# Optimization experiments

Measured on AMD Instinct MI355X. Metric: run time of the kernel, lower is better.

## Reference

```python
import jax, jax.numpy as jnp
import numpy as np

H = 150
PASSES = 5
NSETS = 2
N = 50000
E = 400000
G = 64
SLOPE = 0.01  # torch leaky_relu default


def setup_inputs() -> dict:
    key = jax.random.key(0)
    ks = jax.random.split(key, 20)
    def u(k, shape, fan):
        lim = 1.0 / np.sqrt(fan)
        return jax.random.uniform(k, shape, jnp.float32, -lim, lim)
    return {
        "nodes": jax.random.normal(ks[0], (N, H), jnp.float32),
        "problem_type": jax.random.uniform(ks[1], (G, 1), jnp.float32),
        "edge_W": u(ks[2], (NSETS, H, H), H),
        "edge_b": u(ks[3], (NSETS, H), H),
        "gru_w_ih": u(ks[4], (3 * H, H), H),
        "gru_w_hh": u(ks[5], (3 * H, H), H),
        "gru_b_ih": u(ks[6], (3 * H,), H),
        "gru_b_hh": u(ks[7], (3 * H,), H),
        "fc1_w": u(ks[8], (80, 151), 151),
        "fc1_b": u(ks[9], (80,), 151),
        "fc2_w": u(ks[10], (80, 80), 80),
        "fc2_b": u(ks[11], (80,), 80),
        "fcL_w": u(ks[12], (10, 80), 80),
        "fcL_b": u(ks[13], (10,), 80),
        "edges": jax.random.randint(ks[14], (NSETS, E, 2), 0, N),
        "graph_ids": jnp.sort(jax.random.randint(ks[15], (N,), 0, G)),
        "tbptt": 0,
    }


def _gru_cell(x, h, w_ih, w_hh, b_ih, b_hh):
    gi = x @ w_ih.T + b_ih  # [N, 3H]
    gh = h @ w_hh.T + b_hh
    ir, iz, inn = jnp.split(gi, 3, axis=-1)
    hr, hz, hn = jnp.split(gh, 3, axis=-1)
    r = jax.nn.sigmoid(ir + hr)
    z = jax.nn.sigmoid(iz + hz)
    n = jnp.tanh(inn + r * hn)
    return (1.0 - z) * n + z * h


def reference(nodes, problem_type, edge_W, edge_b, gru_w_ih, gru_w_hh,
              gru_b_ih, gru_b_hh, fc1_w, fc1_b, fc2_w, fc2_b, fcL_w, fcL_b,
              edges, graph_ids, tbptt):
    n_sets = edge_W.shape[0]
    n_graphs = problem_type.shape[0]
    for j in range(PASSES):
        incoming = jnp.zeros_like(nodes)
        for k in range(n_sets):
            src = edges[k, :, 1]
            dst = edges[k, :, 0]
            # NOTE: in the source, the first Linear+leaky_relu result is
            # overwritten; the effective edge message is just the second Linear.
            y = nodes[src] @ edge_W[k].T + edge_b[k]  # [E, H]
            incoming = incoming.at[dst].add(y)
        nodes = _gru_cell(incoming, nodes, gru_w_ih, gru_w_hh, gru_b_ih, gru_b_hh)
        if tbptt == 1 and j < PASSES - 2:
            nodes = jax.lax.stop_gradient(nodes)
    g = jax.ops.segment_sum(nodes, graph_ids, num_segments=n_graphs)  # [G, H]
    g = jnp.log(g)
    g = jnp.where(jnp.isnan(g), 0.0, g)
    g = jax.nn.relu(g)
    x = jnp.concatenate([g, problem_type], axis=1)  # [G, 151]
    x = jax.nn.leaky_relu(x @ fc1_w.T + fc1_b, SLOPE)
    x = jax.nn.leaky_relu(x @ fc2_w.T + fc2_b, SLOPE)
    return x @ fcL_w.T + fcL_b  # [G, 10]
```

## Files before the change

### kernel.cpp

```cpp
#include <hip/hip_runtime.h>
#include <stdint.h>

#define NN 50000
#define H 150
#define NE 400000
#define NG 64
#define NPASS 5
#define KB 480
#define VC 640
#define NRB 391

typedef unsigned short u16;
typedef unsigned int u32;
typedef __attribute__((ext_vector_type(8))) short short8;
typedef __attribute__((ext_vector_type(4))) float float4v;
typedef __attribute__((ext_vector_type(4))) u32 uint4v;

__device__ __forceinline__ u16 f2bf_rn(float x) {
  union { float f; u32 u; } v; v.f = x;
  u32 r = v.u + 0x7fffu + ((v.u >> 16) & 1u);
  return (u16)(r >> 16);
}
__device__ __forceinline__ float bf2f(u16 h) {
  union { u32 u; float f; } v; v.u = ((u32)h) << 16;
  return v.f;
}
__device__ __forceinline__ u32 packf(float v) {
  u16 hi = f2bf_rn(v);
  u16 lo = f2bf_rn(v - bf2f(hi));
  return (u32)hi | ((u32)lo << 16);
}
__device__ __forceinline__ float upk(u32 u) {
  union { u32 u; float f; } a, b;
  a.u = u << 16; b.u = u & 0xffff0000u;
  return a.f + b.f;
}
__device__ __forceinline__ void async16(const void* g, void* l) {
  __builtin_amdgcn_global_load_lds(
      (const __attribute__((address_space(1))) unsigned int*)(uintptr_t)g,
      (__attribute__((address_space(3))) unsigned int*)(uint32_t)(uintptr_t)l,
      16, 0, 0);
}

__global__ void hist_kernel(const int* __restrict__ edges, int* __restrict__ cnt) {
  int id = blockIdx.x * 256 + threadIdx.x;
  if (id >= 2 * NE) return;
  int dst = edges[id * 2];
  int set = id / NE;
  atomicAdd(&cnt[dst * 2 + set], 1);
}

__global__ __launch_bounds__(1024) void scan1_kernel(const int* __restrict__ cnt,
                                                     int* __restrict__ rowptr,
                                                     int* __restrict__ bsum, int n) {
  __shared__ int sd[1024];
  int t = threadIdx.x;
  int idx = blockIdx.x * 1024 + t;
  int v = (idx < n) ? cnt[idx] : 0;
  sd[t] = v;
  __syncthreads();
  for (int off = 1; off < 1024; off <<= 1) {
    int add = (t >= off) ? sd[t - off] : 0;
    __syncthreads();
    sd[t] += add;
    __syncthreads();
  }
  if (idx < n) rowptr[idx] = sd[t] - v;
  if (t == 1023) bsum[blockIdx.x] = sd[1023];
}

__global__ __launch_bounds__(128) void scan2_kernel(const int* __restrict__ bsum,
                                                    int* __restrict__ boff, int nb) {
  __shared__ int sd[128];
  int t = threadIdx.x;
  int v = (t < nb) ? bsum[t] : 0;
  sd[t] = v;
  __syncthreads();
  for (int off = 1; off < 128; off <<= 1) {
    int add = (t >= off) ? sd[t - off] : 0;
    __syncthreads();
    sd[t] += add;
    __syncthreads();
  }
  boff[t] = sd[t] - v;
}

__global__ void scan3_kernel(int* __restrict__ rowptr, const int* __restrict__ boff, int n) {
  int idx = blockIdx.x * 256 + threadIdx.x;
  if (idx < n) rowptr[idx] += boff[idx >> 10];
}

__global__ void total_kernel(int* __restrict__ rowptr, const int* __restrict__ boff, int n, int nb) {
  if (threadIdx.x == 0 && blockIdx.x == 0) rowptr[n] = boff[nb];
}

__global__ void copy_int_kernel(const int* __restrict__ a, int* __restrict__ b, int n) {
  int id = blockIdx.x * 256 + threadIdx.x;
  if (id < n) b[id] = a[id];
}

__global__ void fill_kernel(const int* __restrict__ edges, int* __restrict__ cursor,
                            u16* __restrict__ colbuf) {
  int id = blockIdx.x * 256 + threadIdx.x;
  if (id >= 2 * NE) return;
  int dst = edges[id * 2];
  int src = edges[id * 2 + 1];
  int set = id / NE;
  int pos = atomicAdd(&cursor[dst * 2 + set], 1);
  colbuf[pos] = (u16)src;
}

__global__ void bounds_kernel(const int* __restrict__ gids, int* __restrict__ gstart) {
  int g = threadIdx.x;
  if (g > NG) return;
  int lo = 0, hi = NN;
  while (lo < hi) { int m = (lo + hi) >> 1; if (gids[m] < g) lo = m + 1; else hi = m; }
  gstart[g] = lo;
}

__global__ void build_B_kernel(const float* __restrict__ wih, const float* __restrict__ whh,
                               const float* __restrict__ eW,
                               u16* __restrict__ Bh, u16* __restrict__ Bl) {
  int id = blockIdx.x * 256 + threadIdx.x;
  if (id >= VC * KB) return;
  int v = id / KB, k = id % KB;
  int g = (v >> 4) & 3, c = (v >> 6) * 16 + (v & 15);
  int seg = k / 160, kk = k % 160;
  float val = 0.f;
  if (c < H && kk < H) {
    if (seg < 2) {
      if (g < 3) {
        const float* wr = wih + (size_t)(g * H + c) * H;
        const float* wc = eW + (size_t)seg * H * H + kk;
        float acc = 0.f;
        for (int t = 0; t < H; t++) acc += wr[t] * wc[(size_t)t * H];
        val = acc;
      }
    } else {
      if (g == 0) val = whh[(size_t)c * H + kk];
      else if (g == 1) val = whh[(size_t)(H + c) * H + kk];
      else if (g == 3) val = whh[(size_t)(2 * H + c) * H + kk];
    }
  }
  u16 h = f2bf_rn(val);
  Bh[id] = h;
  Bl[id] = f2bf_rn(val - bf2f(h));
}

__global__ void build_coef_kernel(const float* __restrict__ wih,
                                  const float* __restrict__ eb,
                                  const float* __restrict__ bih, const float* __restrict__ bhh,
                                  float* __restrict__ coefs) {
  int id = threadIdx.x + blockIdx.x * 256;
  if (id >= VC) return;
  int g = id / 160, c = id % 160;
  float u0 = 0.f, u1 = 0.f, bs = 0.f;
  if (c < H) {
    if (g < 3) {
      const float* wr = wih + (size_t)(g * H + c) * H;
      for (int t = 0; t < H; t++) { u0 += wr[t] * eb[t]; u1 += wr[t] * eb[H + t]; }
    }
    if (g == 0) bs = bih[c] + bhh[c];
    else if (g == 1) bs = bih[H + c] + bhh[H + c];
    else if (g == 2) bs = bih[2 * H + c];
    else bs = bhh[2 * H + c];
  }
  coefs[id] = u0;
  coefs[VC + id] = u1;
  coefs[2 * VC + id] = bs;
}

__global__ void init_nodes_kernel(const float* __restrict__ nin,
                                  u32* __restrict__ npkA, u32* __restrict__ npkB) {
  int id = blockIdx.x * 256 + threadIdx.x;
  if (id >= NN * 160) return;
  int r = id / 160, c = id % 160;
  if (c < H) {
    npkA[id] = packf(nin[(size_t)r * H + c]);
  } else {
    npkA[id] = 0;
    npkB[id] = 0;
  }
}

__global__ void pad_S_kernel(u16* __restrict__ Sh, u16* __restrict__ Sl) {
  int id = blockIdx.x * 256 + threadIdx.x;
  if (id >= NN * 20) return;
  int r = id / 20, rem = id % 20;
  int set = rem / 10, t = rem % 10;
  size_t off = (size_t)r * 320 + set * 160 + H + t;
  Sh[off] = 0; Sl[off] = 0;
}

__global__ __launch_bounds__(256) void gather_kernel(
    const u32* __restrict__ npk, const int* __restrict__ rowptr,
    const u16* __restrict__ colbuf, u16* __restrict__ Sh, u16* __restrict__ Sl) {
  int gtid = blockIdx.x * 256 + threadIdx.x;
  int node = gtid >> 6;
  int lane = gtid & 63;
  if (node >= NN) return;
  int s = rowptr[2 * node], mid = rowptr[2 * node + 1], e = rowptr[2 * node + 2];
  int c0 = lane, c1 = lane + 64, c2 = lane + 128;
  bool ok2 = (c2 < H);
  float a0 = 0.f, a1 = 0.f, a2 = 0.f;
  int p = s;
  for (; p + 1 < mid; p += 2) {
    const u32* rA = npk + (size_t)colbuf[p] * 160;
    const u32* rB = npk + (size_t)colbuf[p + 1] * 160;
    u32 xa0 = rA[c0], xa1 = rA[c1];
    u32 xb0 = rB[c0], xb1 = rB[c1];
    u32 xa2 = 0, xb2 = 0;
    if (ok2) { xa2 = rA[c2]; xb2 = rB[c2]; }
    a0 += upk(xa0) + upk(xb0);
    a1 += upk(xa1) + upk(xb1);
    if (ok2) a2 += upk(xa2) + upk(xb2);
  }
  if (p < mid) {
    const u32* rA = npk + (size_t)colbuf[p] * 160;
    a0 += upk(rA[c0]); a1 += upk(rA[c1]); if (ok2) a2 += upk(rA[c2]);
  }
  float b0 = 0.f, b1 = 0.f, b2 = 0.f;
  p = mid;
  for (; p + 1 < e; p += 2) {
    const u32* rA = npk + (size_t)colbuf[p] * 160;
    const u32* rB = npk + (size_t)colbuf[p + 1] * 160;
    u32 xa0 = rA[c0], xa1 = rA[c1];
    u32 xb0 = rB[c0], xb1 = rB[c1];
    u32 xa2 = 0, xb2 = 0;
    if (ok2) { xa2 = rA[c2]; xb2 = rB[c2]; }
    b0 += upk(xa0) + upk(xb0);
    b1 += upk(xa1) + upk(xb1);
    if (ok2) b2 += upk(xa2) + upk(xb2);
  }
  if (p < e) {
    const u32* rA = npk + (size_t)colbuf[p] * 160;
    b0 += upk(rA[c0]); b1 += upk(rA[c1]); if (ok2) b2 += upk(rA[c2]);
  }
  u16* oh = Sh + (size_t)node * 320;
  u16* ol = Sl + (size_t)node * 320;
  u16 h;
  h = f2bf_rn(a0); oh[c0] = h; ol[c0] = f2bf_rn(a0 - bf2f(h));
  h = f2bf_rn(a1); oh[c1] = h; ol[c1] = f2bf_rn(a1 - bf2f(h));
  if (ok2) { h = f2bf_rn(a2); oh[c2] = h; ol[c2] = f2bf_rn(a2 - bf2f(h)); }
  h = f2bf_rn(b0); oh[160 + c0] = h; ol[160 + c0] = f2bf_rn(b0 - bf2f(h));
  h = f2bf_rn(b1); oh[160 + c1] = h; ol[160 + c1] = f2bf_rn(b1 - bf2f(h));
  if (ok2) { h = f2bf_rn(b2); oh[160 + c2] = h; ol[160 + c2] = f2bf_rn(b2 - bf2f(h)); }
}

__global__ __launch_bounds__(256) void gru_gemm_kernel(
    const u16* __restrict__ Sh, const u16* __restrict__ Sl,
    const u32* __restrict__ npkc,
    const u16* __restrict__ Bh, const u16* __restrict__ Bl,
    const float* __restrict__ coefs, const int* __restrict__ rowptr,
    u32* __restrict__ npkn) {
  __shared__ char Abuf[2][16384];
  __shared__ char Bbuf[2][16384];
  const int bid = blockIdx.x;
  const int xcd = bid & 7;
  const int rest = bid >> 3;
  const int ccb = rest % 5;
  const int r0b = (rest / 5) * 8 + xcd;
  if (r0b >= NRB) return;
  const int r0 = r0b * 128;
  const int tid = threadIdx.x;
  const int w = tid >> 6, l = tid & 63;
  const int m = l & 15, quad = l >> 4;
  const int mrow0 = (w & 1) * 64;
  const int nco0 = (w >> 1) * 64;

  float4v acc[4][4];
  #pragma unroll
  for (int mt = 0; mt < 4; mt++)
    #pragma unroll
    for (int j = 0; j < 4; j++) acc[mt][j] = (float4v){0.f, 0.f, 0.f, 0.f};

  auto stage = [&](int kt, char* Ab, char* Bb) {
    if (kt < 10) {
      int koff = kt * 32;
      #pragma unroll
      for (int i = 0; i < 2; i++) {
        int cl = i * 256 + tid;
        int row = cl >> 2;
        int q = (cl & 3) ^ ((row >> 1) & 3);
        int rg = min(r0 + row, NN - 1);
        size_t go = (size_t)rg * 320 + koff + q * 8;
        int lb = i * 4096 + w * 1024;
        async16(Sh + go, Ab + lb);
        async16(Sl + go, Ab + 8192 + lb);
        if (((row >> 4) & 3) != 3) {
          size_t gb = (size_t)(ccb * 128 + row) * KB + koff + q * 8;
          async16(Bh + gb, Bb + lb);
          async16(Bl + gb, Bb + 8192 + lb);
        }
      }
    } else {
      int koff = (kt - 10) * 32;
      #pragma unroll
      for (int i = 0; i < 4; i++) {
        int cl = i * 256 + tid;
        int row = cl >> 3;
        int q = (cl & 7) ^ (row & 7);
        int rg = min(r0 + row, NN - 1);
        async16(npkc + (size_t)rg * 160 + koff + q * 4, Ab + i * 4096 + w * 1024);
      }
      #pragma unroll
      for (int i = 0; i < 2; i++) {
        int cl = i * 256 + tid;
        int row = cl >> 2;
        int q = (cl & 3) ^ ((row >> 1) & 3);
        if (((row >> 4) & 3) != 2) {
          size_t gb = (size_t)(ccb * 128 + row) * KB + 320 + koff + q * 8;
          int lb = i * 4096 + w * 1024;
          async16(Bh + gb, Bb + lb);
          async16(Bl + gb, Bb + 8192 + lb);
        }
      }
    }
  };

  auto compute = [&](int kt, const char* Ab, const char* Bb) {
    if (kt < 10) {
      short8 bh[3], bl[3];
      #pragma unroll
      for (int j = 0; j < 3; j++) {
        int br = nco0 + j * 16 + m;
        int bd = br * 64 + ((quad ^ ((br >> 1) & 3)) * 16);
        bh[j] = *(const short8*)(Bb + bd);
        bl[j] = *(const short8*)(Bb + 8192 + bd);
      }
      #pragma unroll
      for (int mt = 0; mt < 4; mt++) {
        int r = mrow0 + mt * 16 + m;
        int ad = r * 64 + ((quad ^ ((r >> 1) & 3)) * 16);
        short8 ah = *(const short8*)(Ab + ad);
        short8 al = *(const short8*)(Ab + 8192 + ad);
        #pragma unroll
        for (int j = 0; j < 3; j++) {
          acc[mt][j] = __builtin_amdgcn_mfma_f32_16x16x32_bf16(ah, bh[j], acc[mt][j], 0, 0, 0);
          acc[mt][j] = __builtin_amdgcn_mfma_f32_16x16x32_bf16(ah, bl[j], acc[mt][j], 0, 0, 0);
          acc[mt][j] = __builtin_amdgcn_mfma_f32_16x16x32_bf16(al, bh[j], acc[mt][j], 0, 0, 0);
        }
      }
    } else {
      const int jmap[3] = {0, 1, 3};
      short8 bh[3], bl[3];
      #pragma unroll
      for (int jj = 0; jj < 3; jj++) {
        int br = nco0 + jmap[jj] * 16 + m;
        int bd = br * 64 + ((quad ^ ((br >> 1) & 3)) * 16);
        bh[jj] = *(const short8*)(Bb + bd);
        bl[jj] = *(const short8*)(Bb + 8192 + bd);
      }
      #pragma unroll
      for (int mt = 0; mt < 4; mt++) {
        int r = mrow0 + mt * 16 + m;
        uint4v p0 = *(const uint4v*)(Ab + r * 128 + (((2 * quad) ^ (r & 7)) * 16));
        uint4v p1 = *(const uint4v*)(Ab + r * 128 + (((2 * quad + 1) ^ (r & 7)) * 16));
        u32 uu[8] = {p0.x, p0.y, p0.z, p0.w, p1.x, p1.y, p1.z, p1.w};
        short8 ah, al;
        #pragma unroll
        for (int e2 = 0; e2 < 8; e2++) {
          ah[e2] = (short)(uu[e2] & 0xffffu);
          al[e2] = (short)(uu[e2] >> 16);
        }
        #pragma unroll
        for (int jj = 0; jj < 3; jj++) {
          int j = jmap[jj];
          acc[mt][j] = __builtin_amdgcn_mfma_f32_16x16x32_bf16(ah, bh[jj], acc[mt][j], 0, 0, 0);
          acc[mt][j] = __builtin_amdgcn_mfma_f32_16x16x32_bf16(ah, bl[jj], acc[mt][j], 0, 0, 0);
          acc[mt][j] = __builtin_amdgcn_mfma_f32_16x16x32_bf16(al, bh[jj], acc[mt][j], 0, 0, 0);
        }
      }
    }
  };

  stage(0, Abuf[0], Bbuf[0]);
  __syncthreads();
  #pragma unroll 1
  for (int kt = 0; kt < 15; kt++) {
    int cur = kt & 1;
    if (kt + 1 < 15) stage(kt + 1, Abuf[cur ^ 1], Bbuf[cur ^ 1]);
    compute(kt, Abuf[cur], Bbuf[cur]);
    __syncthreads();
  }

  int c = (ccb * 2 + (w >> 1)) * 16 + m;
  if (c >= H) return;
  float u0r = coefs[c],            u0z = coefs[160 + c],
        u0n = coefs[320 + c];
  float u1r = coefs[VC + c],       u1z = coefs[VC + 160 + c],
        u1n = coefs[VC + 320 + c];
  float bsr = coefs[2 * VC + c],   bsz = coefs[2 * VC + 160 + c],
        bsn = coefs[2 * VC + 320 + c], bsh = coefs[2 * VC + 480 + c];
  #pragma unroll
  for (int mt = 0; mt < 4; mt++) {
    #pragma unroll
    for (int i = 0; i < 4; i++) {
      int row = r0 + mrow0 + mt * 16 + quad * 4 + i;
      if (row >= NN) continue;
      float d0 = (float)(rowptr[2 * row + 1] - rowptr[2 * row]);
      float d1 = (float)(rowptr[2 * row + 2] - rowptr[2 * row + 1]);
      float pr = acc[mt][0][i] + d0 * u0r + d1 * u1r + bsr;
      float pz = acc[mt][1][i] + d0 * u0z + d1 * u1z + bsz;
      float pn = acc[mt][2][i] + d0 * u0n + d1 * u1n + bsn;
      float ph = acc[mt][3][i] + bsh;
      float r_g = 1.f / (1.f + __expf(-pr));
      float z_g = 1.f / (1.f + __expf(-pz));
      float narg = pn + r_g * ph;
      float e2 = __expf(2.f * narg);
      float n_g = 1.f - 2.f / (e2 + 1.f);
      float h = upk(npkc[(size_t)row * 160 + c]);
      npkn[(size_t)row * 160 + c] = packf((1.f - z_g) * n_g + z_g * h);
    }
  }
}

__global__ __launch_bounds__(192) void segsum_kernel(const u32* __restrict__ npk,
                                                     const int* __restrict__ gstart,
                                                     float* __restrict__ gsum) {
  int g = blockIdx.x, chunk = blockIdx.y;
  int c = threadIdx.x;
  if (c >= H) return;
  int s = gstart[g], e = gstart[g + 1];
  int len = e - s;
  if (len <= 0) return;
  int per = (len + 3) / 4;
  int rs = s + chunk * per;
  int re = min(e, rs + per);
  if (rs >= re) return;
  float acc = 0.f;
  for (int r = rs; r < re; r++) acc += upk(npk[(size_t)r * 160 + c]);
  atomicAdd(&gsum[g * H + c], acc);
}

__global__ __launch_bounds__(192) void head_kernel(
    const float* __restrict__ gsum, const float* __restrict__ pt,
    const float* __restrict__ fc1_w, const float* __restrict__ fc1_b,
    const float* __restrict__ fc2_w, const float* __restrict__ fc2_b,
    const float* __restrict__ fcL_w, const float* __restrict__ fcL_b,
    float* __restrict__ out) {
  __shared__ float x[151];
  __shared__ float x1[80];
  __shared__ float x2[80];
  int row = blockIdx.x;
  int t = threadIdx.x;
  if (t < 151) {
    float v;
    if (t < H) { float g = gsum[row * H + t]; v = (g > 1.f) ? logf(g) : 0.f; }
    else v = pt[row];
    x[t] = v;
  }
  __syncthreads();
  if (t < 80) {
    float acc = fc1_b[t];
    const float* wrow = fc1_w + t * 151;
    #pragma unroll 4
    for (int k = 0; k < 151; k++) acc += x[k] * wrow[k];
    x1[t] = (acc > 0.f) ? acc : 0.01f * acc;
  }
  __syncthreads();
  if (t < 80) {
    float acc = fc2_b[t];
    const float* wrow = fc2_w + t * 80;
    #pragma unroll 4
    for (int k = 0; k < 80; k++) acc += x1[k] * wrow[k];
    x2[t] = (acc > 0.f) ? acc : 0.01f * acc;
  }
  __syncthreads();
  if (t < 10) {
    float acc = fcL_b[t];
    const float* wrow = fcL_w + t * 80;
    #pragma unroll 4
    for (int k = 0; k < 80; k++) acc += x2[k] * wrow[k];
    out[row * 10 + t] = acc;
  }
}

extern "C" void kernel_launch(void* const* d_in, const int* in_sizes, int n_in,
                              void* d_out, int out_size, void* d_ws, size_t ws_size,
                              hipStream_t stream) {
  const float* nodes_in = (const float*)d_in[0];
  const float* problem_type = (const float*)d_in[1];
  const float* edge_W = (const float*)d_in[2];
  const float* edge_b = (const float*)d_in[3];
  const float* w_ih = (const float*)d_in[4];
  const float* w_hh = (const float*)d_in[5];
  const float* b_ih = (const float*)d_in[6];
  const float* b_hh = (const float*)d_in[7];
  const float* fc1_w = (const float*)d_in[8];
  const float* fc1_b = (const float*)d_in[9];
  const float* fc2_w = (const float*)d_in[10];
  const float* fc2_b = (const float*)d_in[11];
  const float* fcL_w = (const float*)d_in[12];
  const float* fcL_b = (const float*)d_in[13];
  const int* edges = (const int*)d_in[14];
  const int* graph_ids = (const int*)d_in[15];

  char* ws = (char*)d_ws;
  size_t off = 0;
  auto alloc = [&](size_t bytes) -> void* {
    void* p = ws + off;
    off = (off + bytes + 255) & ~(size_t)255;
    return p;
  };
  u32* npkA     = (u32*)alloc((size_t)NN * 160 * 4);
  u32* npkB     = (u32*)alloc((size_t)NN * 160 * 4);
  u16* Sh       = (u16*)alloc((size_t)NN * 320 * 2);
  u16* Sl       = (u16*)alloc((size_t)NN * 320 * 2);
  u16* Bh       = (u16*)alloc((size_t)VC * KB * 2);
  u16* Bl       = (u16*)alloc((size_t)VC * KB * 2);
  float* coefs  = (float*)alloc(3 * VC * 4);
  int* rowptr   = (int*)alloc((2 * NN + 1) * 4);
  int* cursor   = (int*)alloc(2 * NN * 4);
  u16* colbuf   = (u16*)alloc(2ull * NE * 2);
  int* bsum     = (int*)alloc(128 * 4);
  int* boff     = (int*)alloc(128 * 4);
  int* gstart   = (int*)alloc((NG + 1) * 4);
  float* gsum   = (float*)alloc((size_t)NG * H * 4);

  const int n2 = 2 * NN;
  const int nb = (n2 + 1023) / 1024;

  hipMemsetAsync(cursor, 0, n2 * 4, stream);
  hist_kernel<<<(2 * NE + 255) / 256, 256, 0, stream>>>(edges, cursor);
  scan1_kernel<<<nb, 1024, 0, stream>>>(cursor, rowptr, bsum, n2);
  scan2_kernel<<<1, 128, 0, stream>>>(bsum, boff, nb);
  scan3_kernel<<<(n2 + 255) / 256, 256, 0, stream>>>(rowptr, boff, n2);
  total_kernel<<<1, 64, 0, stream>>>(rowptr, boff, n2, nb);
  copy_int_kernel<<<(n2 + 255) / 256, 256, 0, stream>>>(rowptr, cursor, n2);
  fill_kernel<<<(2 * NE + 255) / 256, 256, 0, stream>>>(edges, cursor, colbuf);
  bounds_kernel<<<1, 128, 0, stream>>>(graph_ids, gstart);
  build_B_kernel<<<(VC * KB + 255) / 256, 256, 0, stream>>>(w_ih, w_hh, edge_W, Bh, Bl);
  build_coef_kernel<<<(VC + 255) / 256, 256, 0, stream>>>(w_ih, edge_b, b_ih, b_hh, coefs);
  init_nodes_kernel<<<(NN * 160 + 255) / 256, 256, 0, stream>>>(nodes_in, npkA, npkB);
  pad_S_kernel<<<(NN * 20 + 255) / 256, 256, 0, stream>>>(Sh, Sl);

  const int ngrp = (NRB + 7) / 8;
  u32* nbuf[2] = {npkA, npkB};
  for (int pass = 0; pass < NPASS; pass++) {
    u32* cur = nbuf[pass & 1];
    u32* nxt = nbuf[1 - (pass & 1)];
    gather_kernel<<<(NN * 64 + 255) / 256, 256, 0, stream>>>(cur, rowptr, colbuf, Sh, Sl);
    gru_gemm_kernel<<<ngrp * 5 * 8, 256, 0, stream>>>(
        Sh, Sl, cur, Bh, Bl, coefs, rowptr, nxt);
  }
  u32* fin = nbuf[NPASS & 1];

  hipMemsetAsync(gsum, 0, (size_t)NG * H * 4, stream);
  segsum_kernel<<<dim3(NG, 4), 192, 0, stream>>>(fin, gstart, gsum);
  head_kernel<<<NG, 192, 0, stream>>>(gsum, problem_type, fc1_w, fc1_b, fc2_w, fc2_b,
                                      fcL_w, fcL_b, (float*)d_out);
}
```

Before: 1.168 ms.

## Restructure GRU GEMM k-loop into register-prefetch pipeline with explicit waitcnts

The k-loop of the GRU matmul kernel is split into two specialized loops. Each iteration first loads all LDS fragments into registers, then issues the next-next async stage into the freed buffer, and waits with explicit partial vmcnt counts instead of full __syncthreads. The MFMA block runs at raised wave priority via s_setprio. This overlaps global->LDS copies with MFMA work more tightly, at the cost of more registers and fragile hand-tuned wait counts that depend on each wave's async load counts.

```diff
diff --git a/kernel.cpp b/kernel.cpp
--- a/kernel.cpp
+++ b/kernel.cpp
@@ -318,70 +318,108 @@
     }
   };
 
-  auto compute = [&](int kt, const char* Ab, const char* Bb) {
-    if (kt < 10) {
-      short8 bh[3], bl[3];
+  stage(0, Abuf[0], Bbuf[0]);
+  stage(1, Abuf[1], Bbuf[1]);
+  if (w == 3) { asm volatile("s_waitcnt vmcnt(4)" ::: "memory"); }
+  else        { asm volatile("s_waitcnt vmcnt(8)" ::: "memory"); }
+  __builtin_amdgcn_sched_barrier(0);
+  __builtin_amdgcn_s_barrier();
+
+  #pragma unroll 1
+  for (int kt = 0; kt < 10; kt++) {
+    const char* Ab = Abuf[kt & 1];
+    const char* Bb = Bbuf[kt & 1];
+    short8 bh[3], bl[3], ah[4], al[4];
+    #pragma unroll
+    for (int j = 0; j < 3; j++) {
+      int br = nco0 + j * 16 + m;
+      int bd = br * 64 + ((quad ^ ((br >> 1) & 3)) * 16);
+      bh[j] = *(const short8*)(Bb + bd);
+      bl[j] = *(const short8*)(Bb + 8192 + bd);
+    }
+    #pragma unroll
+    for (int mt = 0; mt < 4; mt++) {
+      int r = mrow0 + mt * 16 + m;
+      int ad = r * 64 + ((quad ^ ((r >> 1) & 3)) * 16);
+      ah[mt] = *(const short8*)(Ab + ad);
+      al[mt] = *(const short8*)(Ab + 8192 + ad);
+    }
+    asm volatile("s_waitcnt lgkmcnt(0)" ::: "memory");
+    __builtin_amdgcn_sched_barrier(0);
+    __builtin_amdgcn_s_barrier();
+    stage(kt + 2, Abuf[kt & 1], Bbuf[kt & 1]);
+    {
+      const int lw = (kt < 8) ? 3 : 2;
+      if (w == lw) { asm volatile("s_waitcnt vmcnt(4)" ::: "memory"); }
+      else         { asm volatile("s_waitcnt vmcnt(8)" ::: "memory"); }
+    }
+    __builtin_amdgcn_sched_barrier(0);
+    __builtin_amdgcn_s_barrier();
+    __builtin_amdgcn_s_setprio(1);
+    #pragma unroll
+    for (int mt = 0; mt < 4; mt++) {
       #pragma unroll
       for (int j = 0; j < 3; j++) {
-        int br = nco0 + j * 16 + m;
-        int bd = br * 64 + ((quad ^ ((br >> 1) & 3)) * 16);
-        bh[j] = *(const short8*)(Bb + bd);
-        bl[j] = *(const short8*)(Bb + 8192 + bd);
-      }
+        acc[mt][j] = __builtin_amdgcn_mfma_f32_16x16x32_bf16(ah[mt], bh[j], acc[mt][j], 0, 0, 0);
+        acc[mt][j] = __builtin_amdgcn_mfma_f32_16x16x32_bf16(ah[mt], bl[j], acc[mt][j], 0, 0, 0);
+        acc[mt][j] = __builtin_amdgcn_mfma_f32_16x16x32_bf16(al[mt], bh[j], acc[mt][j], 0, 0, 0);
+      }
+    }
+    __builtin_amdgcn_s_setprio(0);
+  }
+
+  #pragma unroll 1
+  for (int kt = 10; kt < 15; kt++) {
+    const char* Ab = Abuf[kt & 1];
+    const char* Bb = Bbuf[kt & 1];
+    const int jmap[3] = {0, 1, 3};
+    short8 bh[3], bl[3];
+    #pragma unroll
+    for (int jj = 0; jj < 3; jj++) {
+      int br = nco0 + jmap[jj] * 16 + m;
+      int bd = br * 64 + ((quad ^ ((br >> 1) & 3)) * 16);
+      bh[jj] = *(const short8*)(Bb + bd);
+      bl[jj] = *(const short8*)(Bb + 8192 + bd);
+    }
+    uint4v p0[4], p1[4];
+    #pragma unroll
+    for (int mt = 0; mt < 4; mt++) {
+      int r = mrow0 + mt * 16 + m;
+      p0[mt] = *(const uint4v*)(Ab + r * 128 + (((2 * quad) ^ (r & 7)) * 16));
+      p1[mt] = *(const uint4v*)(Ab + r * 128 + (((2 * quad + 1) ^ (r & 7)) * 16));
+    }
+    asm volatile("s_waitcnt lgkmcnt(0)" ::: "memory");
+    __builtin_amdgcn_sched_barrier(0);
+    __builtin_amdgcn_s_barrier();
+    if (kt + 2 < 15) {
+      stage(kt + 2, Abuf[kt & 1], Bbuf[kt & 1]);
+      if (w == 2) { asm volatile("s_waitcnt vmcnt(4)" ::: "memory"); }
+      else        { asm volatile("s_waitcnt vmcnt(8)" ::: "memory"); }
+    } else {
+      asm volatile("s_waitcnt vmcnt(0)" ::: "memory");
+    }
+    __builtin_amdgcn_sched_barrier(0);
+    __builtin_amdgcn_s_barrier();
+    __builtin_amdgcn_s_setprio(1);
+    #pragma unroll
+    for (int mt = 0; mt < 4; mt++) {
+      u32 uu[8] = {p0[mt].x, p0[mt].y, p0[mt].z, p0[mt].w,
+                   p1[mt].x, p1[mt].y, p1[mt].z, p1[mt].w};
+      short8 ah, al;
       #pragma unroll
-      for (int mt = 0; mt < 4; mt++) {
-        int r = mrow0 + mt * 16 + m;
-        int ad = r * 64 + ((quad ^ ((r >> 1) & 3)) * 16);
-        short8 ah = *(const short8*)(Ab + ad);
-        short8 al = *(const short8*)(Ab + 8192 + ad);
-        #pragma unroll
-        for (int j = 0; j < 3; j++) {
-          acc[mt][j] = __builtin_amdgcn_mfma_f32_16x16x32_bf16(ah, bh[j], acc[mt][j], 0, 0, 0);
-          acc[mt][j] = __builtin_amdgcn_mfma_f32_16x16x32_bf16(ah, bl[j], acc[mt][j], 0, 0, 0);
-          acc[mt][j] = __builtin_amdgcn_mfma_f32_16x16x32_bf16(al, bh[j], acc[mt][j], 0, 0, 0);
-        }
-      }
-    } else {
-      const int jmap[3] = {0, 1, 3};
-      short8 bh[3], bl[3];
+      for (int e2 = 0; e2 < 8; e2++) {
+        ah[e2] = (short)(uu[e2] & 0xffffu);
+        al[e2] = (short)(uu[e2] >> 16);
+      }
       #pragma unroll
       for (int jj = 0; jj < 3; jj++) {
-        int br = nco0 + jmap[jj] * 16 + m;
-        int bd = br * 64 + ((quad ^ ((br >> 1) & 3)) * 16);
-        bh[jj] = *(const short8*)(Bb + bd);
-        bl[jj] = *(const short8*)(Bb + 8192 + bd);
-      }
-      #pragma unroll
-      for (int mt = 0; mt < 4; mt++) {
-        int r = mrow0 + mt * 16 + m;
-        uint4v p0 = *(const uint4v*)(Ab + r * 128 + (((2 * quad) ^ (r & 7)) * 16));
-        uint4v p1 = *(const uint4v*)(Ab + r * 128 + (((2 * quad + 1) ^ (r & 7)) * 16));
-        u32 uu[8] = {p0.x, p0.y, p0.z, p0.w, p1.x, p1.y, p1.z, p1.w};
-        short8 ah, al;
-        #pragma unroll
-        for (int e2 = 0; e2 < 8; e2++) {
-          ah[e2] = (short)(uu[e2] & 0xffffu);
-          al[e2] = (short)(uu[e2] >> 16);
-        }
-        #pragma unroll
-        for (int jj = 0; jj < 3; jj++) {
-          int j = jmap[jj];
-          acc[mt][j] = __builtin_amdgcn_mfma_f32_16x16x32_bf16(ah, bh[jj], acc[mt][j], 0, 0, 0);
-          acc[mt][j] = __builtin_amdgcn_mfma_f32_16x16x32_bf16(ah, bl[jj], acc[mt][j], 0, 0, 0);
-          acc[mt][j] = __builtin_amdgcn_mfma_f32_16x16x32_bf16(al, bh[jj], acc[mt][j], 0, 0, 0);
-        }
-      }
-    }
-  };
-
-  stage(0, Abuf[0], Bbuf[0]);
-  __syncthreads();
-  #pragma unroll 1
-  for (int kt = 0; kt < 15; kt++) {
-    int cur = kt & 1;
-    if (kt + 1 < 15) stage(kt + 1, Abuf[cur ^ 1], Bbuf[cur ^ 1]);
-    compute(kt, Abuf[cur], Bbuf[cur]);
-    __syncthreads();
+        int j = jmap[jj];
+        acc[mt][j] = __builtin_amdgcn_mfma_f32_16x16x32_bf16(ah, bh[jj], acc[mt][j], 0, 0, 0);
+        acc[mt][j] = __builtin_amdgcn_mfma_f32_16x16x32_bf16(ah, bl[jj], acc[mt][j], 0, 0, 0);
+        acc[mt][j] = __builtin_amdgcn_mfma_f32_16x16x32_bf16(al, bh[jj], acc[mt][j], 0, 0, 0);
+      }
+    }
+    __builtin_amdgcn_s_setprio(0);
   }
 
   int c = (ccb * 2 + (w >> 1)) * 16 + m;
```

Result: no change. 1.161 ms (-0.7%).

## Pack gather output as hi/lo pairs, split gather per set, software-pipeline GEMM

Applied to the files above, without the earlier changes.

The gather kernel now assigns one wavefront per (node, edge set) instead of per node. It writes packed u32 hi/lo bf16 pairs into a single interleaved buffer, replacing the separate Sh/Sl arrays. The GRU GEMM loop is fully unrolled with templates and runs a deeper pipeline: it stages two tiles ahead, uses explicit vmcnt/lgkmcnt waits and raw barriers, prefetches LDS fragments into registers before each MFMA step, and raises wave priority during the MFMAs. This aims to raise gather parallelism, unify the A-tile load path, and overlap global loads and LDS reads with MFMA work, at the cost of more registers and hand-tuned wait counts that could be fragile.

```diff
diff --git a/kernel.cpp b/kernel.cpp
--- a/kernel.cpp
+++ b/kernel.cpp
@@ -183,28 +183,28 @@
   }
 }
 
-__global__ void pad_S_kernel(u16* __restrict__ Sh, u16* __restrict__ Sl) {
+__global__ void pad_S_kernel(u32* __restrict__ Snp) {
   int id = blockIdx.x * 256 + threadIdx.x;
   if (id >= NN * 20) return;
   int r = id / 20, rem = id % 20;
   int set = rem / 10, t = rem % 10;
-  size_t off = (size_t)r * 320 + set * 160 + H + t;
-  Sh[off] = 0; Sl[off] = 0;
+  Snp[(size_t)r * 320 + set * 160 + H + t] = 0;
 }
 
 __global__ __launch_bounds__(256) void gather_kernel(
     const u32* __restrict__ npk, const int* __restrict__ rowptr,
-    const u16* __restrict__ colbuf, u16* __restrict__ Sh, u16* __restrict__ Sl) {
+    const u16* __restrict__ colbuf, u32* __restrict__ Snp) {
   int gtid = blockIdx.x * 256 + threadIdx.x;
-  int node = gtid >> 6;
+  int wid = gtid >> 6;
+  if (wid >= 2 * NN) return;
+  int node = wid >> 1, set = wid & 1;
   int lane = gtid & 63;
-  if (node >= NN) return;
-  int s = rowptr[2 * node], mid = rowptr[2 * node + 1], e = rowptr[2 * node + 2];
+  int s = rowptr[2 * node + set], e = rowptr[2 * node + set + 1];
   int c0 = lane, c1 = lane + 64, c2 = lane + 128;
   bool ok2 = (c2 < H);
   float a0 = 0.f, a1 = 0.f, a2 = 0.f;
   int p = s;
-  for (; p + 1 < mid; p += 2) {
+  for (; p + 1 < e; p += 2) {
     const u32* rA = npk + (size_t)colbuf[p] * 160;
     const u32* rB = npk + (size_t)colbuf[p + 1] * 160;
     u32 xa0 = rA[c0], xa1 = rA[c1];
@@ -215,42 +215,132 @@
     a1 += upk(xa1) + upk(xb1);
     if (ok2) a2 += upk(xa2) + upk(xb2);
   }
-  if (p < mid) {
+  if (p < e) {
     const u32* rA = npk + (size_t)colbuf[p] * 160;
     a0 += upk(rA[c0]); a1 += upk(rA[c1]); if (ok2) a2 += upk(rA[c2]);
   }
-  float b0 = 0.f, b1 = 0.f, b2 = 0.f;
-  p = mid;
-  for (; p + 1 < e; p += 2) {
-    const u32* rA = npk + (size_t)colbuf[p] * 160;
-    const u32* rB = npk + (size_t)colbuf[p + 1] * 160;
-    u32 xa0 = rA[c0], xa1 = rA[c1];
-    u32 xb0 = rB[c0], xb1 = rB[c1];
-    u32 xa2 = 0, xb2 = 0;
-    if (ok2) { xa2 = rA[c2]; xb2 = rB[c2]; }
-    b0 += upk(xa0) + upk(xb0);
-    b1 += upk(xa1) + upk(xb1);
-    if (ok2) b2 += upk(xa2) + upk(xb2);
-  }
-  if (p < e) {
-    const u32* rA = npk + (size_t)colbuf[p] * 160;
-    b0 += upk(rA[c0]); b1 += upk(rA[c1]); if (ok2) b2 += upk(rA[c2]);
-  }
-  u16* oh = Sh + (size_t)node * 320;
-  u16* ol = Sl + (size_t)node * 320;
-  u16 h;
-  h = f2bf_rn(a0); oh[c0] = h; ol[c0] = f2bf_rn(a0 - bf2f(h));
-  h = f2bf_rn(a1); oh[c1] = h; ol[c1] = f2bf_rn(a1 - bf2f(h));
-  if (ok2) { h = f2bf_rn(a2); oh[c2] = h; ol[c2] = f2bf_rn(a2 - bf2f(h)); }
-  h = f2bf_rn(b0); oh[160 + c0] = h; ol[160 + c0] = f2bf_rn(b0 - bf2f(h));
-  h = f2bf_rn(b1); oh[160 + c1] = h; ol[160 + c1] = f2bf_rn(b1 - bf2f(h));
-  if (ok2) { h = f2bf_rn(b2); oh[160 + c2] = h; ol[160 + c2] = f2bf_rn(b2 - bf2f(h)); }
+  u32* o = Snp + (size_t)node * 320 + set * 160;
+  o[c0] = packf(a0);
+  o[c1] = packf(a1);
+  if (ok2) o[c2] = packf(a2);
+}
+
+
+template<int KT>
+__device__ __forceinline__ void stage_fn(
+    const u32* __restrict__ Snp, const u32* __restrict__ npkc,
+    const u16* __restrict__ Bhp, const u16* __restrict__ Blp,
+    char* Ab, char* Bb, int tid, int w, int r0, int ccb) {
+  #pragma unroll
+  for (int i = 0; i < 4; i++) {
+    int cl = i * 256 + tid;
+    int row = cl >> 3;
+    int q = (cl & 7) ^ (row & 7);
+    int rg = min(r0 + row, NN - 1);
+    if constexpr (KT < 10)
+      async16(Snp + (size_t)rg * 320 + KT * 32 + q * 4, Ab + i * 4096 + w * 1024);
+    else
+      async16(npkc + (size_t)rg * 160 + (KT - 10) * 32 + q * 4, Ab + i * 4096 + w * 1024);
+  }
+  constexpr int koffB = (KT < 10) ? KT * 32 : 320 + (KT - 10) * 32;
+  constexpr int skipg = (KT < 10) ? 3 : 2;
+  #pragma unroll
+  for (int i = 0; i < 2; i++) {
+    int cl = i * 256 + tid;
+    int row = cl >> 2;
+    int q = (cl & 3) ^ ((row >> 1) & 3);
+    if (((row >> 4) & 3) != skipg) {
+      size_t gb = (size_t)(ccb * 128 + row) * KB + koffB + q * 8;
+      int lb = i * 4096 + w * 1024;
+      async16(Bhp + gb, Bb + lb);
+      async16(Blp + gb, Bb + 8192 + lb);
+    }
+  }
+}
+
+template<int KTn>
+__device__ __forceinline__ void read_frags_fn(
+    const char* Ab, const char* Bb, int m, int quad, int mrow0, int nco0,
+    uint4v (&A0)[4], uint4v (&A1)[4], short8 (&RBh)[3], short8 (&RBl)[3]) {
+  #pragma unroll
+  for (int jj = 0; jj < 3; jj++) {
+    const int jsel = (jj == 2) ? ((KTn < 10) ? 2 : 3) : jj;
+    int br = nco0 + jsel * 16 + m;
+    int bd = br * 64 + ((quad ^ ((br >> 1) & 3)) * 16);
+    RBh[jj] = *(const short8*)(Bb + bd);
+    RBl[jj] = *(const short8*)(Bb + 8192 + bd);
+  }
+  #pragma unroll
+  for (int mt = 0; mt < 4; mt++) {
+    int r = mrow0 + mt * 16 + m;
+    A0[mt] = *(const uint4v*)(Ab + r * 128 + (((2 * quad) ^ (r & 7)) * 16));
+    A1[mt] = *(const uint4v*)(Ab + r * 128 + (((2 * quad + 1) ^ (r & 7)) * 16));
+  }
+}
+
+template<int KT>
+__device__ __forceinline__ void mfma_fn(
+    const uint4v (&A0)[4], const uint4v (&A1)[4],
+    const short8 (&MBh)[3], const short8 (&MBl)[3], float4v (&acc)[4][4]) {
+  #pragma unroll
+  for (int mt = 0; mt < 4; mt++) {
+    u32 uu[8] = {A0[mt].x, A0[mt].y, A0[mt].z, A0[mt].w,
+                 A1[mt].x, A1[mt].y, A1[mt].z, A1[mt].w};
+    short8 ah, al;
+    #pragma unroll
+    for (int e2 = 0; e2 < 8; e2++) {
+      ah[e2] = (short)(uu[e2] & 0xffffu);
+      al[e2] = (short)(uu[e2] >> 16);
+    }
+    #pragma unroll
+    for (int jj = 0; jj < 3; jj++) {
+      const int J = (KT < 10) ? jj : ((jj == 2) ? 3 : jj);
+      acc[mt][J] = __builtin_amdgcn_mfma_f32_16x16x32_bf16(ah, MBh[jj], acc[mt][J], 0, 0, 0);
+      acc[mt][J] = __builtin_amdgcn_mfma_f32_16x16x32_bf16(ah, MBl[jj], acc[mt][J], 0, 0, 0);
+      acc[mt][J] = __builtin_amdgcn_mfma_f32_16x16x32_bf16(al, MBh[jj], acc[mt][J], 0, 0, 0);
+    }
+  }
+}
+
+template<int KT>
+__device__ __forceinline__ void gemm_step(
+    const u32* __restrict__ Snp, const u32* __restrict__ npkc,
+    const u16* __restrict__ Bhp, const u16* __restrict__ Blp,
+    char (&Abuf)[2][16384], char (&Bbuf)[2][16384],
+    int tid, int w, int m, int quad, int mrow0, int nco0, int r0, int ccb,
+    uint4v (&A0)[2][4], uint4v (&A1)[2][4], short8 (&FBh)[2][3], short8 (&FBl)[2][3],
+    float4v (&acc)[4][4]) {
+  constexpr int cur = KT & 1;
+  constexpr int nxt = cur ^ 1;
+  if constexpr (KT + 2 <= 14)
+    stage_fn<KT + 2>(Snp, npkc, Bhp, Blp, Abuf[cur], Bbuf[cur], tid, w, r0, ccb);
+  if constexpr (KT + 1 <= 14) {
+    if constexpr (KT + 2 <= 14) {
+      constexpr int lw = (KT + 2 < 10) ? 3 : 2;
+      if (w == lw) { asm volatile("s_waitcnt vmcnt(4)" ::: "memory"); }
+      else         { asm volatile("s_waitcnt vmcnt(8)" ::: "memory"); }
+    } else {
+      asm volatile("s_waitcnt vmcnt(0)" ::: "memory");
+    }
+    __builtin_amdgcn_sched_barrier(0);
+    __builtin_amdgcn_s_barrier();
+    read_frags_fn<KT + 1>(Abuf[nxt], Bbuf[nxt], m, quad, mrow0, nco0,
+                          A0[nxt], A1[nxt], FBh[nxt], FBl[nxt]);
+    __builtin_amdgcn_sched_barrier(0);
+  }
+  __builtin_amdgcn_s_setprio(1);
+  mfma_fn<KT>(A0[cur], A1[cur], FBh[cur], FBl[cur], acc);
+  __builtin_amdgcn_s_setprio(0);
+  if constexpr (KT + 3 <= 14) {
+    asm volatile("s_waitcnt lgkmcnt(0)" ::: "memory");
+    __builtin_amdgcn_sched_barrier(0);
+    __builtin_amdgcn_s_barrier();
+  }
 }
 
 __global__ __launch_bounds__(256) void gru_gemm_kernel(
-    const u16* __restrict__ Sh, const u16* __restrict__ Sl,
-    const u32* __restrict__ npkc,
-    const u16* __restrict__ Bh, const u16* __restrict__ Bl,
+    const u32* __restrict__ Snp, const u32* __restrict__ npkc,
+    const u16* __restrict__ Bhp, const u16* __restrict__ Blp,
     const float* __restrict__ coefs, const int* __restrict__ rowptr,
     u32* __restrict__ npkn) {
   __shared__ char Abuf[2][16384];
@@ -274,115 +364,27 @@
     #pragma unroll
     for (int j = 0; j < 4; j++) acc[mt][j] = (float4v){0.f, 0.f, 0.f, 0.f};
 
-  auto stage = [&](int kt, char* Ab, char* Bb) {
-    if (kt < 10) {
-      int koff = kt * 32;
-      #pragma unroll
-      for (int i = 0; i < 2; i++) {
-        int cl = i * 256 + tid;
-        int row = cl >> 2;
-        int q = (cl & 3) ^ ((row >> 1) & 3);
-        int rg = min(r0 + row, NN - 1);
-        size_t go = (size_t)rg * 320 + koff + q * 8;
-        int lb = i * 4096 + w * 1024;
-        async16(Sh + go, Ab + lb);
-        async16(Sl + go, Ab + 8192 + lb);
-        if (((row >> 4) & 3) != 3) {
-          size_t gb = (size_t)(ccb * 128 + row) * KB + koff + q * 8;
-          async16(Bh + gb, Bb + lb);
-          async16(Bl + gb, Bb + 8192 + lb);
-        }
-      }
-    } else {
-      int koff = (kt - 10) * 32;
-      #pragma unroll
-      for (int i = 0; i < 4; i++) {
-        int cl = i * 256 + tid;
-        int row = cl >> 3;
-        int q = (cl & 7) ^ (row & 7);
-        int rg = min(r0 + row, NN - 1);
-        async16(npkc + (size_t)rg * 160 + koff + q * 4, Ab + i * 4096 + w * 1024);
-      }
-      #pragma unroll
-      for (int i = 0; i < 2; i++) {
-        int cl = i * 256 + tid;
-        int row = cl >> 2;
-        int q = (cl & 3) ^ ((row >> 1) & 3);
-        if (((row >> 4) & 3) != 2) {
-          size_t gb = (size_t)(ccb * 128 + row) * KB + 320 + koff + q * 8;
-          int lb = i * 4096 + w * 1024;
-          async16(Bh + gb, Bb + lb);
-          async16(Bl + gb, Bb + 8192 + lb);
-        }
-      }
-    }
-  };
-
-  auto compute = [&](int kt, const char* Ab, const char* Bb) {
-    if (kt < 10) {
-      short8 bh[3], bl[3];
-      #pragma unroll
-      for (int j = 0; j < 3; j++) {
-        int br = nco0 + j * 16 + m;
-        int bd = br * 64 + ((quad ^ ((br >> 1) & 3)) * 16);
-        bh[j] = *(const short8*)(Bb + bd);
-        bl[j] = *(const short8*)(Bb + 8192 + bd);
-      }
-      #pragma unroll
-      for (int mt = 0; mt < 4; mt++) {
-        int r = mrow0 + mt * 16 + m;
-        int ad = r * 64 + ((quad ^ ((r >> 1) & 3)) * 16);
-        short8 ah = *(const short8*)(Ab + ad);
-        short8 al = *(const short8*)(Ab + 8192 + ad);
-        #pragma unroll
-        for (int j = 0; j < 3; j++) {
-          acc[mt][j] = __builtin_amdgcn_mfma_f32_16x16x32_bf16(ah, bh[j], acc[mt][j], 0, 0, 0);
-          acc[mt][j] = __builtin_amdgcn_mfma_f32_16x16x32_bf16(ah, bl[j], acc[mt][j], 0, 0, 0);
-          acc[mt][j] = __builtin_amdgcn_mfma_f32_16x16x32_bf16(al, bh[j], acc[mt][j], 0, 0, 0);
-        }
-      }
-    } else {
-      const int jmap[3] = {0, 1, 3};
-      short8 bh[3], bl[3];
-      #pragma unroll
-      for (int jj = 0; jj < 3; jj++) {
-        int br = nco0 + jmap[jj] * 16 + m;
-        int bd = br * 64 + ((quad ^ ((br >> 1) & 3)) * 16);
-        bh[jj] = *(const short8*)(Bb + bd);
-        bl[jj] = *(const short8*)(Bb + 8192 + bd);
-      }
-      #pragma unroll
-      for (int mt = 0; mt < 4; mt++) {
-        int r = mrow0 + mt * 16 + m;
-        uint4v p0 = *(const uint4v*)(Ab + r * 128 + (((2 * quad) ^ (r & 7)) * 16));
-        uint4v p1 = *(const uint4v*)(Ab + r * 128 + (((2 * quad + 1) ^ (r & 7)) * 16));
-        u32 uu[8] = {p0.x, p0.y, p0.z, p0.w, p1.x, p1.y, p1.z, p1.w};
-        short8 ah, al;
-        #pragma unroll
-        for (int e2 = 0; e2 < 8; e2++) {
-          ah[e2] = (short)(uu[e2] & 0xffffu);
-          al[e2] = (short)(uu[e2] >> 16);
-        }
-        #pragma unroll
-        for (int jj = 0; jj < 3; jj++) {
-          int j = jmap[jj];
-          acc[mt][j] = __builtin_amdgcn_mfma_f32_16x16x32_bf16(ah, bh[jj], acc[mt][j], 0, 0, 0);
-          acc[mt][j] = __builtin_amdgcn_mfma_f32_16x16x32_bf16(ah, bl[jj], acc[mt][j], 0, 0, 0);
-          acc[mt][j] = __builtin_amdgcn_mfma_f32_16x16x32_bf16(al, bh[jj], acc[mt][j], 0, 0, 0);
-        }
-      }
-    }
-  };
-
-  stage(0, Abuf[0], Bbuf[0]);
-  __syncthreads();
-  #pragma unroll 1
-  for (int kt = 0; kt < 15; kt++) {
-    int cur = kt & 1;
-    if (kt + 1 < 15) stage(kt + 1, Abuf[cur ^ 1], Bbuf[cur ^ 1]);
-    compute(kt, Abuf[cur], Bbuf[cur]);
-    __syncthreads();
-  }
+  uint4v A0[2][4], A1[2][4];
+  short8 FBh[2][3], FBl[2][3];
+
+  stage_fn<0>(Snp, npkc, Bhp, Blp, Abuf[0], Bbuf[0], tid, w, r0, ccb);
+  stage_fn<1>(Snp, npkc, Bhp, Blp, Abuf[1], Bbuf[1], tid, w, r0, ccb);
+  if (w == 3) { asm volatile("s_waitcnt vmcnt(4)" ::: "memory"); }
+  else        { asm volatile("s_waitcnt vmcnt(8)" ::: "memory"); }
+  __builtin_amdgcn_sched_barrier(0);
+  __builtin_amdgcn_s_barrier();
+  read_frags_fn<0>(Abuf[0], Bbuf[0], m, quad, mrow0, nco0,
+                   A0[0], A1[0], FBh[0], FBl[0]);
+  asm volatile("s_waitcnt lgkmcnt(0)" ::: "memory");
+  __builtin_amdgcn_sched_barrier(0);
+  __builtin_amdgcn_s_barrier();
+
+  #define STEP(K) gemm_step<K>(Snp, npkc, Bhp, Blp, Abuf, Bbuf, tid, w, m, quad, \
+                               mrow0, nco0, r0, ccb, A0, A1, FBh, FBl, acc)
+  STEP(0);  STEP(1);  STEP(2);  STEP(3);  STEP(4);
+  STEP(5);  STEP(6);  STEP(7);  STEP(8);  STEP(9);
+  STEP(10); STEP(11); STEP(12); STEP(13); STEP(14);
+  #undef STEP
 
   int c = (ccb * 2 + (w >> 1)) * 16 + m;
   if (c >= H) return;
@@ -505,8 +507,7 @@
   };
   u32* npkA     = (u32*)alloc((size_t)NN * 160 * 4);
   u32* npkB     = (u32*)alloc((size_t)NN * 160 * 4);
-  u16* Sh       = (u16*)alloc((size_t)NN * 320 * 2);
-  u16* Sl       = (u16*)alloc((size_t)NN * 320 * 2);
+  u32* Snp      = (u32*)alloc((size_t)NN * 320 * 4);
   u16* Bh       = (u16*)alloc((size_t)VC * KB * 2);
   u16* Bl       = (u16*)alloc((size_t)VC * KB * 2);
   float* coefs  = (float*)alloc(3 * VC * 4);
@@ -533,16 +534,16 @@
   build_B_kernel<<<(VC * KB + 255) / 256, 256, 0, stream>>>(w_ih, w_hh, edge_W, Bh, Bl);
   build_coef_kernel<<<(VC + 255) / 256, 256, 0, stream>>>(w_ih, edge_b, b_ih, b_hh, coefs);
   init_nodes_kernel<<<(NN * 160 + 255) / 256, 256, 0, stream>>>(nodes_in, npkA, npkB);
-  pad_S_kernel<<<(NN * 20 + 255) / 256, 256, 0, stream>>>(Sh, Sl);
+  pad_S_kernel<<<(NN * 20 + 255) / 256, 256, 0, stream>>>(Snp);
 
   const int ngrp = (NRB + 7) / 8;
   u32* nbuf[2] = {npkA, npkB};
   for (int pass = 0; pass < NPASS; pass++) {
     u32* cur = nbuf[pass & 1];
     u32* nxt = nbuf[1 - (pass & 1)];
-    gather_kernel<<<(NN * 64 + 255) / 256, 256, 0, stream>>>(cur, rowptr, colbuf, Sh, Sl);
+    gather_kernel<<<(2 * NN * 64 + 255) / 256, 256, 0, stream>>>(cur, rowptr, colbuf, Snp);
     gru_gemm_kernel<<<ngrp * 5 * 8, 256, 0, stream>>>(
-        Sh, Sl, cur, Bh, Bl, coefs, rowptr, nxt);
+        Snp, cur, Bh, Bl, coefs, rowptr, nxt);
   }
   u32* fin = nbuf[NPASS & 1];
 
```

New measurement: 1.171 ms. About the same (+0.3%).
